# Optimization experiments

Measured on AMD Instinct MI355X. Metric: run time of the kernel, lower is better.

Reference implementation:

```python
import jax, jax.numpy as jnp
import numpy as np
from jax import lax

ALPHA = 4.0  # spikingjelly Sigmoid surrogate default alpha
EPS = 1e-5

@jax.custom_vjp
def _spike(x):
    return (x >= 0.0).astype(x.dtype)

def _spike_fwd(x):
    return (x >= 0.0).astype(x.dtype), x

def _spike_bwd(x, g):
    s = jax.nn.sigmoid(ALPHA * x)
    return (g * ALPHA * s * (1.0 - s),)

_spike.defvjp(_spike_fwd, _spike_bwd)

def _lif(x, tau=2.0, vth=1.0):
    # MultiStepLIFNode: v += (x - v)/tau (v_reset=0), hard reset, detach_reset
    def step(v, xt):
        v = v + (xt - v) / tau
        s = _spike(v - vth)
        v = (1.0 - lax.stop_gradient(s)) * v
        return v, s
    _, s = lax.scan(step, jnp.zeros_like(x[0]), x)
    return s

def _negif(x, vth=1.0):
    # MultiStepNegIFNode: integrate-and-fire with +/- spikes (signed wavelet coeffs), soft reset
    def step(v, xt):
        v = v + xt
        s = _spike(v - vth) - _spike(-v - vth)
        v = v - lax.stop_gradient(s) * vth
        return v, s
    _, s = lax.scan(step, jnp.zeros_like(x[0]), x)
    return s

def _haar_matrix(n):
    # orthonormal Haar transform matrix, n a power of 2
    h = np.array([[1.0]])
    while h.shape[0] < n:
        top = np.kron(h, [1.0, 1.0])
        bot = np.kron(np.eye(h.shape[0]), [1.0, -1.0])
        h = np.concatenate([top, bot], axis=0) / np.sqrt(2.0)
    return jnp.asarray(h, dtype=jnp.float32)

def _bn(x, w, b, m, v):
    # eval-mode BatchNorm2d over NCHW
    inv = w / jnp.sqrt(v + EPS)
    return x * inv[None, :, None, None] + (b - m * inv)[None, :, None, None]

def _conv(x, w, b, pad):
    y = lax.conv_general_dilated(x, w, (1, 1), [(pad, pad), (pad, pad)],
                                 dimension_numbers=('NCHW', 'OIHW', 'NCHW'))
    return y + b[None, :, None, None]

def _fatm(x, haar_weight, conv1_w, conv1_b, conv2_w, conv2_b,
          bn_weight, bn_bias, bn_mean, bn_var, vth=1.0):
    T, B, C, H, W = x.shape
    nb, bs = haar_weight.shape[0], haar_weight.shape[1]
    Q = _haar_matrix(H)
    identity = x
    xs = _lif(x)                                                   # [T,B,C,H,W] binary spikes
    # Haar2DForward: Q X Q^T over spatial dims, then NegIF spiking
    haar = _negif(jnp.einsum('ij,tbcjk,lk->tbcil', Q, xs, Q), vth)
    haar = _bn(haar.reshape(T * B, C, H, W), bn_weight[0], bn_bias[0], bn_mean[0], bn_var[0])
    haar = _lif(haar.reshape(T, B, C, H, W))
    # block-diagonal channel mixing (num_blocks tiny bs x bs GEMMs per pixel)
    h = haar.reshape(T * B, nb, bs, H, W)
    h = jnp.einsum('nbdhw,bdk->nbkhw', h, haar_weight)
    haar = _bn(h.reshape(T * B, C, H, W), bn_weight[1], bn_bias[1], bn_mean[1], bn_var[1])
    # Haar2DInverse: Q^T X Q, then NegIF spiking
    haar = _negif(jnp.einsum('ji,tbcjk,kl->tbcil', Q, haar.reshape(T, B, C, H, W), Q), vth)
    haar = _bn(haar.reshape(T * B, C, H, W), bn_weight[2], bn_bias[2], bn_mean[2], bn_var[2])
    haar = haar.reshape(T, B, C, H, W)
    # conv branch on spikes, grouped over blocks via batch folding
    xr = xs.reshape(T * B * nb, bs, H, W)
    c1 = _conv(xr, conv1_w, conv1_b, 0)
    c1 = _bn(c1.reshape(T * B, C, H, W), bn_weight[3], bn_bias[3], bn_mean[3], bn_var[3]).reshape(T, B, C, H, W)
    c2 = _conv(xr, conv2_w, conv2_b, 1)
    c2 = _bn(c2.reshape(T * B, C, H, W), bn_weight[4], bn_bias[4], bn_mean[4], bn_var[4]).reshape(T, B, C, H, W)
    return haar + c1 + c2 + identity

def setup_inputs():
    key = jax.random.key(0)
    ks = jax.random.split(key, 10)
    T, B, C, H, W = 4, 8, 512, 32, 32
    nb = 16
    bs = C // nb
    return {
        'x': jax.random.normal(ks[0], (T, B, C, H, W), jnp.float32),
        'haar_weight': 0.02 * jax.random.normal(ks[1], (nb, bs, bs), jnp.float32),
        'conv1_w': jax.random.normal(ks[2], (bs, bs, 1, 1), jnp.float32) / np.sqrt(bs),
        'conv1_b': 0.01 * jax.random.normal(ks[3], (bs,), jnp.float32),
        'conv2_w': jax.random.normal(ks[4], (bs, bs, 3, 3), jnp.float32) / np.sqrt(bs * 9.0),
        'conv2_b': 0.01 * jax.random.normal(ks[5], (bs,), jnp.float32),
        'bn_weight': 1.0 + 0.1 * jax.random.normal(ks[6], (5, C), jnp.float32),
        'bn_bias': 0.1 * jax.random.normal(ks[7], (5, C), jnp.float32),
        'bn_mean': 0.1 * jax.random.normal(ks[8], (5, C), jnp.float32),
        'bn_var': 0.5 + jax.random.uniform(ks[9], (5, C), dtype=jnp.float32),
    }

def reference(x, haar_weight, conv1_w, conv1_b, conv2_w, conv2_b,
              bn_weight, bn_bias, bn_mean, bn_var):
    return _fatm(x, haar_weight, conv1_w, conv1_b, conv2_w, conv2_b,
                 bn_weight, bn_bias, bn_mean, bn_var)
```

## Files before the change

### kernel.cpp

```cpp
#include <hip/hip_runtime.h>
#include <math.h>


#define T_    4
#define B_    8
#define C_    512
#define HW_   1024
#define CHW_  524288
#define BCHW_ 4194304
#define NB_   16
#define EPS_  1e-5f
#define QSTR  36

typedef _Float16 half8_t __attribute__((ext_vector_type(8)));
typedef float f32x16_t __attribute__((ext_vector_type(16)));

__global__ void k_build_q(float* __restrict__ q) {
  int idx = threadIdx.x;
  int k = idx >> 5, j = idx & 31;
  double m = 1.0;
  if (k == 0) {
    for (int s = 0; s < 5; ++s) m /= sqrt(2.0);
    q[idx] = (float)m;
    return;
  }
  int p = 31 - __clz(k);
  for (int s = 0; s < 5 - p; ++s) m /= sqrt(2.0);
  int L = 32 >> p;
  int st = (k - (1 << p)) * L;
  int half = L >> 1;
  float v = 0.0f;
  if (j >= st && j < st + half)       v = (float)m;
  else if (j >= st + half && j < st + L) v = -(float)m;
  q[idx] = v;
}

__global__ __launch_bounds__(256) void k_lif_x(const float* __restrict__ x,
                                               unsigned char* __restrict__ xs) {
  size_t i4 = ((size_t)blockIdx.x * 256 + threadIdx.x) * 4;
  float v[4] = {0.f, 0.f, 0.f, 0.f};
  for (int t = 0; t < T_; ++t) {
    float4 xv = *(const float4*)(x + (size_t)t * BCHW_ + i4);
    float xa[4] = {xv.x, xv.y, xv.z, xv.w};
    unsigned char sb[4];
#pragma unroll
    for (int e = 0; e < 4; ++e) {
      v[e] += (xa[e] - v[e]) * 0.5f;
      bool sp = v[e] >= 1.0f;
      sb[e] = sp ? 1 : 0;
      if (sp) v[e] = 0.0f;
    }
    uchar4 s; s.x = sb[0]; s.y = sb[1]; s.z = sb[2]; s.w = sb[3];
    *(uchar4*)(xs + (size_t)t * BCHW_ + i4) = s;
  }
}

__global__ __launch_bounds__(256) void k_haar_fwd(
    const unsigned char* __restrict__ xs, const float* __restrict__ qg,
    const float* __restrict__ bnw, const float* __restrict__ bnb,
    const float* __restrict__ bnm, const float* __restrict__ bnv,
    unsigned char* __restrict__ h1) {
  __shared__ __align__(16) float QT[32 * QSTR];
  __shared__ __align__(16) float Xs[4][32 * QSTR];
  __shared__ __align__(16) float Tt[4][32 * QSTR];
  const int tid = threadIdx.x;
  for (int e2 = tid; e2 < 1024; e2 += 256) {
    int i = e2 >> 5, j = e2 & 31;
    QT[j * QSTR + i] = qg[e2];
  }
  const int im = tid >> 6;
  const int e  = tid & 63;
  const int i0 = (e >> 3) * 4;
  const int c0 = (e & 7) * 4;
  const int gc = blockIdx.x * 4 + im;
  const int c  = gc & 511;
  const float inv0 = bnw[c] / sqrtf(bnv[c] + EPS_);
  const float bet0 = __fsub_rn(bnb[c], __fmul_rn(bnm[c], inv0));
  const size_t base = (size_t)(gc >> 9) * CHW_ + (size_t)c * HW_;
  float vn[4][4], vl[4][4];
#pragma unroll
  for (int r = 0; r < 4; ++r)
#pragma unroll
    for (int q = 0; q < 4; ++q) { vn[r][q] = 0.f; vl[r][q] = 0.f; }
  __syncthreads();
  for (int t = 0; t < T_; ++t) {
    const uchar4* sp = (const uchar4*)(xs + (size_t)t * BCHW_ + base + e * 16);
#pragma unroll
    for (int q = 0; q < 4; ++q) {
      uchar4 s4 = sp[q];
      int px = e * 16 + q * 4;
      float4 f;
      f.x = (float)s4.x; f.y = (float)s4.y; f.z = (float)s4.z; f.w = (float)s4.w;
      *(float4*)&Xs[im][(px >> 5) * QSTR + (px & 31)] = f;
    }
    __syncthreads();
    float a[4][4];
#pragma unroll
    for (int r = 0; r < 4; ++r)
#pragma unroll
      for (int q = 0; q < 4; ++q) a[r][q] = 0.f;
    for (int j = 0; j < 32; ++j) {
      float4 qv = *(const float4*)&QT[j * QSTR + i0];
      float4 xv = *(const float4*)&Xs[im][j * QSTR + c0];
      float qa[4] = {qv.x, qv.y, qv.z, qv.w};
      float xa[4] = {xv.x, xv.y, xv.z, xv.w};
#pragma unroll
      for (int r = 0; r < 4; ++r)
#pragma unroll
        for (int q = 0; q < 4; ++q) a[r][q] = fmaf(qa[r], xa[q], a[r][q]);
    }
#pragma unroll
    for (int q = 0; q < 4; ++q) {
      float4 f; f.x = a[0][q]; f.y = a[1][q]; f.z = a[2][q]; f.w = a[3][q];
      *(float4*)&Tt[im][(c0 + q) * QSTR + i0] = f;
    }
    __syncthreads();
    float y[4][4];
#pragma unroll
    for (int r = 0; r < 4; ++r)
#pragma unroll
      for (int q = 0; q < 4; ++q) y[r][q] = 0.f;
    for (int k = 0; k < 32; ++k) {
      float4 tv = *(const float4*)&Tt[im][k * QSTR + i0];
      float4 qv = *(const float4*)&QT[k * QSTR + c0];
      float ta[4] = {tv.x, tv.y, tv.z, tv.w};
      float qa[4] = {qv.x, qv.y, qv.z, qv.w};
#pragma unroll
      for (int r = 0; r < 4; ++r)
#pragma unroll
        for (int q = 0; q < 4; ++q) y[r][q] = fmaf(ta[r], qa[q], y[r][q]);
    }
#pragma unroll
    for (int r = 0; r < 4; ++r) {
      unsigned char sb[4];
#pragma unroll
      for (int q = 0; q < 4; ++q) {
        vn[r][q] += y[r][q];
        float s = 0.f;
        if (vn[r][q] >= 1.0f) s = 1.0f;
        else if (vn[r][q] <= -1.0f) s = -1.0f;
        vn[r][q] -= s;
        float bv = __fadd_rn(__fmul_rn(s, inv0), bet0);
        vl[r][q] += (bv - vl[r][q]) * 0.5f;
        bool spk = vl[r][q] >= 1.0f;
        sb[q] = spk ? 1 : 0;
        if (spk) vl[r][q] = 0.f;
      }
      uchar4 so; so.x = sb[0]; so.y = sb[1]; so.z = sb[2]; so.w = sb[3];
      *(uchar4*)(h1 + (size_t)t * BCHW_ + base + (size_t)((i0 + r) * 32 + c0)) = so;
    }
  }
}

__global__ __launch_bounds__(256) void k_mix(
    const unsigned char* __restrict__ h1, const float* __restrict__ hwt,
    const float* __restrict__ bnw, const float* __restrict__ bnb,
    const float* __restrict__ bnm, const float* __restrict__ bnv,
    float* __restrict__ outm) {
  __shared__ unsigned char S[32 * 1024];
  __shared__ float Wt[1024];
  const int n = blockIdx.x;
  const int blk = blockIdx.y;
  const int tid = threadIdx.x;
  for (int e = tid; e < 1024; e += 256) Wt[e] = hwt[blk * 1024 + e];
  const uint4* src = (const uint4*)(h1 + (size_t)n * CHW_ + (size_t)blk * 32 * HW_);
  uint4* dst = (uint4*)S;
  for (int e = tid; e < 2048; e += 256) dst[e] = src[e];
  __syncthreads();
  const int p0 = tid * 4;
  for (int k = 0; k < 32; ++k) {
    const int c = blk * 32 + k;
    const float inv = bnw[C_ + c] / sqrtf(bnv[C_ + c] + EPS_);
    const float bet = __fsub_rn(bnb[C_ + c], __fmul_rn(bnm[C_ + c], inv));
    float a0 = 0.f, a1 = 0.f, a2 = 0.f, a3 = 0.f;
    for (int d = 0; d < 32; ++d) {
      const float w = Wt[d * 32 + k];
      const unsigned int sp = *(const unsigned int*)(S + d * 1024 + p0);
      a0 = fmaf((float)(sp & 255u), w, a0);
      a1 = fmaf((float)((sp >> 8) & 255u), w, a1);
      a2 = fmaf((float)((sp >> 16) & 255u), w, a2);
      a3 = fmaf((float)((sp >> 24) & 255u), w, a3);
    }
    float4 o;
    o.x = __fadd_rn(__fmul_rn(a0, inv), bet);
    o.y = __fadd_rn(__fmul_rn(a1, inv), bet);
    o.z = __fadd_rn(__fmul_rn(a2, inv), bet);
    o.w = __fadd_rn(__fmul_rn(a3, inv), bet);
    *(float4*)(outm + (size_t)n * CHW_ + (size_t)c * HW_ + p0) = o;
  }
}

__global__ __launch_bounds__(256) void k_haar_inv(
    const float* __restrict__ qg,
    const float* __restrict__ bnw, const float* __restrict__ bnb,
    const float* __restrict__ bnm, const float* __restrict__ bnv,
    float* out) {
  __shared__ __align__(16) float Qn[32 * QSTR];
  __shared__ __align__(16) float Xs[4][32 * QSTR];
  __shared__ __align__(16) float Tt[4][32 * QSTR];
  const int tid = threadIdx.x;
  for (int e2 = tid; e2 < 1024; e2 += 256) {
    int i = e2 >> 5, j = e2 & 31;
    Qn[i * QSTR + j] = qg[e2];
  }
  const int im = tid >> 6;
  const int e  = tid & 63;
  const int i0 = (e >> 3) * 4;
  const int c0 = (e & 7) * 4;
  const int gc = blockIdx.x * 4 + im;
  const int c  = gc & 511;
  const float inv2 = bnw[2 * C_ + c] / sqrtf(bnv[2 * C_ + c] + EPS_);
  const float bet2 = __fsub_rn(bnb[2 * C_ + c], __fmul_rn(bnm[2 * C_ + c], inv2));
  const size_t base = (size_t)(gc >> 9) * CHW_ + (size_t)c * HW_;
  float vn[4][4];
#pragma unroll
  for (int r = 0; r < 4; ++r)
#pragma unroll
    for (int q = 0; q < 4; ++q) vn[r][q] = 0.f;
  __syncthreads();
  for (int t = 0; t < T_; ++t) {
    const float4* sp = (const float4*)(out + (size_t)t * BCHW_ + base + e * 16);
#pragma unroll
    for (int q = 0; q < 4; ++q) {
      float4 f = sp[q];
      int px = e * 16 + q * 4;
      *(float4*)&Xs[im][(px >> 5) * QSTR + (px & 31)] = f;
    }
    __syncthreads();
    float a[4][4];
#pragma unroll
    for (int r = 0; r < 4; ++r)
#pragma unroll
      for (int q = 0; q < 4; ++q) a[r][q] = 0.f;
    for (int j = 0; j < 32; ++j) {
      float4 qv = *(const float4*)&Qn[j * QSTR + i0];
      float4 xv = *(const float4*)&Xs[im][j * QSTR + c0];
      float qa[4] = {qv.x, qv.y, qv.z, qv.w};
      float xa[4] = {xv.x, xv.y, xv.z, xv.w};
#pragma unroll
      for (int r = 0; r < 4; ++r)
#pragma unroll
        for (int q = 0; q < 4; ++q) a[r][q] = fmaf(qa[r], xa[q], a[r][q]);
    }
#pragma unroll
    for (int q = 0; q < 4; ++q) {
      float4 f; f.x = a[0][q]; f.y = a[1][q]; f.z = a[2][q]; f.w = a[3][q];
      *(float4*)&Tt[im][(c0 + q) * QSTR + i0] = f;
    }
    __syncthreads();
    float y[4][4];
#pragma unroll
    for (int r = 0; r < 4; ++r)
#pragma unroll
      for (int q = 0; q < 4; ++q) y[r][q] = 0.f;
    for (int k = 0; k < 32; ++k) {
      float4 tv = *(const float4*)&Tt[im][k * QSTR + i0];
      float4 qv = *(const float4*)&Qn[k * QSTR + c0];
      float ta[4] = {tv.x, tv.y, tv.z, tv.w};
      float qa[4] = {qv.x, qv.y, qv.z, qv.w};
#pragma unroll
      for (int r = 0; r < 4; ++r)
#pragma unroll
        for (int q = 0; q < 4; ++q) y[r][q] = fmaf(ta[r], qa[q], y[r][q]);
    }
#pragma unroll
    for (int r = 0; r < 4; ++r) {
      float res[4];
#pragma unroll
      for (int q = 0; q < 4; ++q) {
        vn[r][q] += y[r][q];
        float s = 0.f;
        if (vn[r][q] >= 1.0f) s = 1.0f;
        else if (vn[r][q] <= -1.0f) s = -1.0f;
        vn[r][q] -= s;
        res[q] = __fadd_rn(__fmul_rn(s, inv2), bet2);
      }
      float4 ov; ov.x = res[0]; ov.y = res[1]; ov.z = res[2]; ov.w = res[3];
      *(float4*)(out + (size_t)t * BCHW_ + base + (size_t)((i0 + r) * 32 + c0)) = ov;
    }
  }
}

#define XSTR_ 80
#define YSTR_ (34 * XSTR_)
#define SROWS_ 18
__global__ __launch_bounds__(256) void k_conv_mfma(
    const unsigned char* __restrict__ xs, const float* __restrict__ x,
    const float* __restrict__ w1, const float* __restrict__ b1,
    const float* __restrict__ w2, const float* __restrict__ b2,
    const float* __restrict__ bnw, const float* __restrict__ bnb,
    const float* __restrict__ bnm, const float* __restrict__ bnv,
    float* out) {
  __shared__ __align__(16) unsigned char S[SROWS_ * 34 * XSTR_];
  const int tid = threadIdx.x;
  const int n = blockIdx.x, blk = blockIdx.y, y0 = blockIdx.z * 16;
  const int wv = tid >> 6, ln = tid & 63;
  for (int i = tid; i < SROWS_ * 34 * XSTR_ / 4; i += 256)
    ((unsigned int*)S)[i] = 0u;
  __syncthreads();
  {
    const int ic4 = ln >> 3, px4 = ln & 7;
    const size_t gb = (size_t)n * CHW_ + (size_t)(blk * 32 + ic4 * 4) * HW_;
    for (int row = wv; row < SROWS_; row += 4) {
      int gy = y0 - 1 + row;
      if (gy < 0 || gy > 31) continue;
      const size_t rb = gb + (size_t)gy * 32 + px4 * 4;
      unsigned int d0 = *(const unsigned int*)(xs + rb);
      unsigned int d1 = *(const unsigned int*)(xs + rb + HW_);
      unsigned int d2 = *(const unsigned int*)(xs + rb + 2 * HW_);
      unsigned int d3 = *(const unsigned int*)(xs + rb + 3 * HW_);
#pragma unroll
      for (int p = 0; p < 4; ++p) {
        unsigned int q = ((d0 >> (8 * p)) & 0xFFu)
                       | (((d1 >> (8 * p)) & 0xFFu) << 8)
                       | (((d2 >> (8 * p)) & 0xFFu) << 16)
                       | (((d3 >> (8 * p)) & 0xFFu) << 24);
        unsigned int lo = ((q & 0xFFu) | ((q & 0xFF00u) << 8)) * 0x3C00u;
        unsigned int hi = (((q >> 16) & 0xFFu) | (((q >> 16) & 0xFF00u) << 8)) * 0x3C00u;
        uint2 wv2; wv2.x = lo; wv2.y = hi;
        *(uint2*)&S[row * YSTR_ + (px4 * 4 + p + 1) * XSTR_ + ic4 * 8] = wv2;
      }
    }
  }
  const int oc_a = ln & 31, hh = ln >> 5;
  half8_t A2[18], A1[2];
#pragma unroll
  for (int tap = 0; tap < 9; ++tap) {
#pragma unroll
    for (int kh = 0; kh < 2; ++kh) {
      half8_t a;
#pragma unroll
      for (int j = 0; j < 8; ++j) {
        int ic = kh * 16 + hh * 8 + j;
        a[j] = (_Float16)w2[(oc_a * 32 + ic) * 9 + tap];
      }
      A2[tap * 2 + kh] = a;
    }
  }
#pragma unroll
  for (int kh = 0; kh < 2; ++kh) {
    half8_t a;
#pragma unroll
    for (int j = 0; j < 8; ++j)
      a[j] = (_Float16)w1[oc_a * 32 + kh * 16 + hh * 8 + j];
    A1[kh] = a;
  }
  float p3[16], p4[16], pcc[16];
#pragma unroll
  for (int r = 0; r < 16; ++r) {
    const int oc = (r & 3) + 8 * (r >> 2) + 4 * hh;
    const int c = blk * 32 + oc;
    const float i3 = bnw[3 * C_ + c] / sqrtf(bnv[3 * C_ + c] + EPS_);
    const float e3 = __fsub_rn(bnb[3 * C_ + c], __fmul_rn(bnm[3 * C_ + c], i3));
    const float i4 = bnw[4 * C_ + c] / sqrtf(bnv[4 * C_ + c] + EPS_);
    const float e4 = __fsub_rn(bnb[4 * C_ + c], __fmul_rn(bnm[4 * C_ + c], i4));
    p3[r] = i3; p4[r] = i4;
    pcc[r] = __fadd_rn(__fadd_rn(__fmul_rn(b1[oc], i3), e3),
                       __fadd_rn(__fmul_rn(b2[oc], i4), e4));
  }
  __syncthreads();
  const int px = ln & 31;
  for (int i = 0; i < 4; ++i) {
    const int ly = wv * 4 + i;
    f32x16_t ac1, ac2;
#pragma unroll
    for (int r = 0; r < 16; ++r) { ac1[r] = 0.f; ac2[r] = 0.f; }
#pragma unroll
    for (int tap = 0; tap < 9; ++tap) {
      const int dy = tap / 3, dx = tap % 3;
#pragma unroll
      for (int kh = 0; kh < 2; ++kh) {
        half8_t b = *(const half8_t*)&S[(ly + dy) * YSTR_ + (px + dx) * XSTR_
                                        + kh * 32 + hh * 16];
        ac2 = __builtin_amdgcn_mfma_f32_32x32x16_f16(A2[tap * 2 + kh], b, ac2, 0, 0, 0);
        if (tap == 4)
          ac1 = __builtin_amdgcn_mfma_f32_32x32x16_f16(A1[kh], b, ac1, 0, 0, 0);
      }
    }
    const int y = y0 + ly;
#pragma unroll
    for (int r = 0; r < 16; ++r) {
      const int oc = (r & 3) + 8 * (r >> 2) + 4 * hh;
      const size_t off = (size_t)n * CHW_ + (size_t)(blk * 32 + oc) * HW_
                       + (size_t)(y * 32 + px);
      const float hv = out[off];
      const float xv = x[off];
      float t1 = __fadd_rn(hv, __fmul_rn(ac1[r], p3[r]));
      float t2 = __fadd_rn(t1, __fmul_rn(ac2[r], p4[r]));
      out[off] = __fadd_rn(__fadd_rn(t2, pcc[r]), xv);
    }
  }
}

extern "C" void kernel_launch(void* const* d_in, const int* in_sizes, int n_in,
                              void* d_out, int out_size, void* d_ws, size_t ws_size,
                              hipStream_t stream) {
  (void)in_sizes; (void)n_in; (void)out_size; (void)ws_size;
  const float* x   = (const float*)d_in[0];
  const float* hwt = (const float*)d_in[1];
  const float* w1  = (const float*)d_in[2];
  const float* b1  = (const float*)d_in[3];
  const float* w2  = (const float*)d_in[4];
  const float* b2  = (const float*)d_in[5];
  const float* bnw = (const float*)d_in[6];
  const float* bnb = (const float*)d_in[7];
  const float* bnm = (const float*)d_in[8];
  const float* bnv = (const float*)d_in[9];
  float* out = (float*)d_out;

  float* qg = (float*)d_ws;
  unsigned char* xs = (unsigned char*)d_ws + 4096;
  unsigned char* h1 = xs + (size_t)T_ * BCHW_;

  k_build_q<<<1, 1024, 0, stream>>>(qg);
  k_lif_x<<<BCHW_ / 1024, 256, 0, stream>>>(x, xs);
  k_haar_fwd<<<(B_ * C_) / 4, 256, 0, stream>>>(xs, qg, bnw, bnb, bnm, bnv, h1);
  k_mix<<<dim3(T_ * B_, NB_), 256, 0, stream>>>(h1, hwt, bnw, bnb, bnm, bnv, out);
  k_haar_inv<<<(B_ * C_) / 4, 256, 0, stream>>>(qg, bnw, bnb, bnm, bnv, out);
  k_conv_mfma<<<dim3(T_ * B_, NB_, 2), 256, 0, stream>>>(xs, x, w1, b1, w2, b2,
                                                         bnw, bnb, bnm, bnv, out);
}
```

Measured before the change: 399.4 us.

## Shrink conv row tile, raise occupancy, prefetch epilogue loads before MFMA

The conv kernel now covers 8 output rows per block instead of 16. This doubles the grid, shrinks shared memory, and adds a three-wave occupancy hint. Only the halo border columns are zeroed instead of the whole shared buffer, and out-of-range rows are written as zeros directly. The epilogue loads of out and x are issued before the MFMA loop to hide their latency. In exchange, each block loads more halo rows relative to its output and register pressure goes up.

```diff
diff --git a/kernel.cpp b/kernel.cpp
--- a/kernel.cpp
+++ b/kernel.cpp
@@ -283,8 +283,8 @@
 
 #define XSTR_ 80
 #define YSTR_ (34 * XSTR_)
-#define SROWS_ 18
-__global__ __launch_bounds__(256) void k_conv_mfma(
+#define SROWS_ 10
+__global__ __launch_bounds__(256, 3) void k_conv_mfma(
     const unsigned char* __restrict__ xs, const float* __restrict__ x,
     const float* __restrict__ w1, const float* __restrict__ b1,
     const float* __restrict__ w2, const float* __restrict__ b2,
@@ -293,22 +293,27 @@
     float* out) {
   __shared__ __align__(16) unsigned char S[SROWS_ * 34 * XSTR_];
   const int tid = threadIdx.x;
-  const int n = blockIdx.x, blk = blockIdx.y, y0 = blockIdx.z * 16;
+  const int n = blockIdx.x, blk = blockIdx.y, y0 = blockIdx.z * 8;
   const int wv = tid >> 6, ln = tid & 63;
-  for (int i = tid; i < SROWS_ * 34 * XSTR_ / 4; i += 256)
-    ((unsigned int*)S)[i] = 0u;
-  __syncthreads();
+  for (int e = tid; e < 400; e += 256) {
+    int row = e / 40, rem = e % 40;
+    int colbase = (rem < 20) ? 0 : 33 * XSTR_;
+    ((unsigned int*)&S[row * YSTR_ + colbase])[rem % 20] = 0u;
+  }
   {
     const int ic4 = ln >> 3, px4 = ln & 7;
     const size_t gb = (size_t)n * CHW_ + (size_t)(blk * 32 + ic4 * 4) * HW_;
     for (int row = wv; row < SROWS_; row += 4) {
-      int gy = y0 - 1 + row;
-      if (gy < 0 || gy > 31) continue;
-      const size_t rb = gb + (size_t)gy * 32 + px4 * 4;
-      unsigned int d0 = *(const unsigned int*)(xs + rb);
-      unsigned int d1 = *(const unsigned int*)(xs + rb + HW_);
-      unsigned int d2 = *(const unsigned int*)(xs + rb + 2 * HW_);
-      unsigned int d3 = *(const unsigned int*)(xs + rb + 3 * HW_);
+      const int gy = y0 - 1 + row;
+      const bool ok = (gy >= 0) && (gy <= 31);
+      unsigned int d0 = 0u, d1 = 0u, d2 = 0u, d3 = 0u;
+      if (ok) {
+        const size_t rb = gb + (size_t)gy * 32 + px4 * 4;
+        d0 = *(const unsigned int*)(xs + rb);
+        d1 = *(const unsigned int*)(xs + rb + HW_);
+        d2 = *(const unsigned int*)(xs + rb + 2 * HW_);
+        d3 = *(const unsigned int*)(xs + rb + 3 * HW_);
+      }
 #pragma unroll
       for (int p = 0; p < 4; ++p) {
         unsigned int q = ((d0 >> (8 * p)) & 0xFFu)
@@ -360,8 +365,18 @@
   }
   __syncthreads();
   const int px = ln & 31;
-  for (int i = 0; i < 4; ++i) {
-    const int ly = wv * 4 + i;
+  for (int i = 0; i < 2; ++i) {
+    const int ly = wv * 2 + i;
+    const int y = y0 + ly;
+    float hva[16], xva[16];
+#pragma unroll
+    for (int r = 0; r < 16; ++r) {
+      const int oc = (r & 3) + 8 * (r >> 2) + 4 * hh;
+      const size_t off = (size_t)n * CHW_ + (size_t)(blk * 32 + oc) * HW_
+                       + (size_t)(y * 32 + px);
+      hva[r] = out[off];
+      xva[r] = x[off];
+    }
     f32x16_t ac1, ac2;
 #pragma unroll
     for (int r = 0; r < 16; ++r) { ac1[r] = 0.f; ac2[r] = 0.f; }
@@ -377,17 +392,14 @@
           ac1 = __builtin_amdgcn_mfma_f32_32x32x16_f16(A1[kh], b, ac1, 0, 0, 0);
       }
     }
-    const int y = y0 + ly;
 #pragma unroll
     for (int r = 0; r < 16; ++r) {
       const int oc = (r & 3) + 8 * (r >> 2) + 4 * hh;
       const size_t off = (size_t)n * CHW_ + (size_t)(blk * 32 + oc) * HW_
                        + (size_t)(y * 32 + px);
-      const float hv = out[off];
-      const float xv = x[off];
-      float t1 = __fadd_rn(hv, __fmul_rn(ac1[r], p3[r]));
+      float t1 = __fadd_rn(hva[r], __fmul_rn(ac1[r], p3[r]));
       float t2 = __fadd_rn(t1, __fmul_rn(ac2[r], p4[r]));
-      out[off] = __fadd_rn(__fadd_rn(t2, pcc[r]), xv);
+      out[off] = __fadd_rn(__fadd_rn(t2, pcc[r]), xva[r]);
     }
   }
 }
@@ -417,6 +429,6 @@
   k_haar_fwd<<<(B_ * C_) / 4, 256, 0, stream>>>(xs, qg, bnw, bnb, bnm, bnv, h1);
   k_mix<<<dim3(T_ * B_, NB_), 256, 0, stream>>>(h1, hwt, bnw, bnb, bnm, bnv, out);
   k_haar_inv<<<(B_ * C_) / 4, 256, 0, stream>>>(qg, bnw, bnb, bnm, bnv, out);
-  k_conv_mfma<<<dim3(T_ * B_, NB_, 2), 256, 0, stream>>>(xs, x, w1, b1, w2, b2,
+  k_conv_mfma<<<dim3(T_ * B_, NB_, 4), 256, 0, stream>>>(xs, x, w1, b1, w2, b2,
                                                          bnw, bnb, bnm, bnv, out);
 }
```

Result: slower. 506.8 us (+26.9%).
